# Optimization experiments

Measured on AMD Instinct MI355X. Metric: run time of the kernel, lower is better.

Reference implementation:

```python
import jax, jax.numpy as jnp
import numpy as np

C, H, W, D, M = 64, 512, 512, 4, 16


def setup_inputs() -> dict:
    key = jax.random.key(0)
    ks = jax.random.split(key, 9)
    scale = (1.0 / (C * C)) ** 0.5
    return {
        "q": jax.random.normal(ks[0], (1, 1, H, W), jnp.float32),
        "proj_w": jax.random.normal(ks[1], (C, 1, 1, 1), jnp.float32),
        "proj_b": jax.random.normal(ks[2], (C, 1, 1), jnp.float32) * 0.01,
        "spec_wr": jax.random.normal(ks[3], (D, C, C, M, M), jnp.float32) * scale,
        "spec_wi": jax.random.normal(ks[4], (D, C, C, M, M), jnp.float32) * scale,
        "w_w": jax.random.normal(ks[5], (D, C, C, 1, 1), jnp.float32) * (1.0 / C ** 0.5),
        "w_b": jax.random.normal(ks[6], (D, C, 1, 1), jnp.float32) * 0.01,
        "final_w": jax.random.normal(ks[7], (1, C, 1, 1), jnp.float32) * (1.0 / C ** 0.5),
        "final_b": jax.random.normal(ks[8], (1, 1, 1), jnp.float32) * 0.01,
    }


def _spectral(x, wr, wi, m):
    # x: (C,H,W). FFT2 -> contract low modes -> zero-pad -> iFFT2, take real part.
    Cin, Hh, Ww = x.shape
    x_ft = jnp.fft.fft2(x, axes=(-2, -1))  # (C,H,W) complex
    w = (wr + 1j * wi).astype(x_ft.dtype)  # (Cin,Cout,m,m)
    out_sub = jnp.einsum('imn,iomn->omn', x_ft[:, :m, :m], w)
    out_ft = jnp.zeros((wr.shape[1], Hh, Ww), dtype=x_ft.dtype).at[:, :m, :m].set(out_sub)
    return jnp.fft.ifft2(out_ft, axes=(-2, -1)).real


def reference(q, proj_w, proj_b, spec_wr, spec_wi, w_w, w_b, final_w, final_b):
    m = spec_wr.shape[-1]
    depth = spec_wr.shape[0]
    x = q[0].astype(jnp.float32)  # (C_in,H,W) -- batch must be 1
    # 1x1 conv lift
    x = jnp.einsum('oi,ihw->ohw', proj_w[:, :, 0, 0], x) + proj_b
    for d in range(depth):
        x_spec = _spectral(x, spec_wr[d], spec_wi[d], m)
        x_local = jnp.einsum('oi,ihw->ohw', w_w[d, :, :, 0, 0], x) + w_b[d]
        x = jax.nn.gelu(x_spec + x_local)
    x = jnp.einsum('oi,ihw->ohw', final_w[:, :, 0, 0], x) + final_b
    return x[None]  # re-add batch dim
```

## Files before the change

### kernel.cpp

```cpp
#include <hip/hip_runtime.h>
#include <cmath>

#define CC 64
#define HH 512
#define WWID 512
#define HWSZ (HH*WWID)
#define DEPTH 4

typedef __attribute__((ext_vector_type(8))) short short8;
typedef __attribute__((ext_vector_type(4))) float floatx4;

__device__ inline unsigned short f2bf(float f){
  unsigned int u = __float_as_uint(f);
  u += 0x7FFF + ((u >> 16) & 1);
  return (unsigned short)(u >> 16);
}
__device__ inline float bf2f(unsigned short h){
  return __uint_as_float(((unsigned int)h) << 16);
}

__global__ void k_init(const float* __restrict__ ww,
                       float* __restrict__ ctab, float* __restrict__ stab,
                       unsigned short* __restrict__ trigBh, unsigned short* __restrict__ trigBl,
                       unsigned short* __restrict__ trigTh, unsigned short* __restrict__ trigTl,
                       unsigned short* __restrict__ Whi, unsigned short* __restrict__ Wlo,
                       float4* __restrict__ Xfz){
  if (blockIdx.x < 32) Xfz[blockIdx.x*256 + threadIdx.x] = make_float4(0.f,0.f,0.f,0.f);
  int idx = blockIdx.x*256 + threadIdx.x;
  if (idx < 8192){
    int pos = idx >> 4, k = idx & 15;
    int r = (pos * k) & 511;
    double ang = (2.0 * 3.14159265358979323846 / 512.0) * (double)r;
    float c = (float)cos(ang), s = (float)sin(ang);
    ctab[idx] = c;  stab[idx] = s;
    unsigned short ch = f2bf(c), sh = f2bf(s);
    unsigned short cl = f2bf(c - bf2f(ch)), sl = f2bf(s - bf2f(sh));
    trigBh[pos*32 + 2*k]     = ch;  trigBl[pos*32 + 2*k]     = cl;
    trigBh[pos*32 + 2*k + 1] = sh;  trigBl[pos*32 + 2*k + 1] = sl;
    trigTh[(2*k)*512 + pos]   = ch;  trigTl[(2*k)*512 + pos]   = cl;
    trigTh[(2*k+1)*512 + pos] = sh;  trigTl[(2*k+1)*512 + pos] = sl;
  } else {
    int t = idx - 8192;
    float v = ww[t];
    unsigned short h = f2bf(v);
    Whi[t] = h;  Wlo[t] = f2bf(v - bf2f(h));
  }
}

#define APITCH 136
#define XPITCH 33
template<int LIFT>
__global__ __launch_bounds__(256) void k_dftw(const float* __restrict__ x,
    const float* __restrict__ qsrc, const float* __restrict__ pw, const float* __restrict__ pb,
    const unsigned short* __restrict__ trigTh, const unsigned short* __restrict__ trigTl,
    const float* __restrict__ ctab, const float* __restrict__ stab,
    float* __restrict__ Xfa, float4* __restrict__ Yz){
  if (blockIdx.x < 32) Yz[blockIdx.x*256 + threadIdx.x] = make_float4(0.f,0.f,0.f,0.f);

  __shared__ unsigned short Ahs[64*APITCH], Als[64*APITCH];
  __shared__ unsigned short Bhs[32*APITCH], Bls[32*APITCH];
  __shared__ float X1s[64*XPITCH];
  int row0 = blockIdx.x * 64;
  int i  = row0 >> 9;
  int h0 = row0 & 511;
  int t = threadIdx.x;
  int g = t >> 6, lm = t & 15, lq = (t >> 4) & 3;
  float pa = 0.f, pbv = 0.f;
  if (LIFT){ pa = pw[i]; pbv = pb[i]; }

  floatx4 acc[2] = {{0.f,0.f,0.f,0.f},{0.f,0.f,0.f,0.f}};

  for (int kc = 0; kc < 4; ++kc){
    {
      int r = t >> 2, qq = t & 3;
      const float4* src4 = LIFT
        ? (const float4*)(qsrc + (size_t)(h0 + r)*512 + kc*128 + qq*32)
        : (const float4*)(x    + (size_t)(row0 + r)*512 + kc*128 + qq*32);
      unsigned int* dh = (unsigned int*)&Ahs[r*APITCH + qq*32];
      unsigned int* dl = (unsigned int*)&Als[r*APITCH + qq*32];
      #pragma unroll
      for (int u = 0; u < 8; ++u){
        float4 v = src4[u];
        if (LIFT){
          v.x = fmaf(pa, v.x, pbv); v.y = fmaf(pa, v.y, pbv);
          v.z = fmaf(pa, v.z, pbv); v.w = fmaf(pa, v.w, pbv);
        }
        unsigned short h0_ = f2bf(v.x), h1 = f2bf(v.y), h2 = f2bf(v.z), h3 = f2bf(v.w);
        dh[u*2]   = (unsigned)h0_ | ((unsigned)h1 << 16);
        dh[u*2+1] = (unsigned)h2 | ((unsigned)h3 << 16);
        unsigned short g0 = f2bf(v.x - bf2f(h0_)), g1 = f2bf(v.y - bf2f(h1));
        unsigned short g2 = f2bf(v.z - bf2f(h2)), g3 = f2bf(v.w - bf2f(h3));
        dl[u*2]   = (unsigned)g0 | ((unsigned)g1 << 16);
        dl[u*2+1] = (unsigned)g2 | ((unsigned)g3 << 16);
      }
    }
    {
      int j = t >> 3, qq = t & 7;
      const unsigned int* sh = (const unsigned int*)trigTh + j*256 + kc*64 + qq*8;
      const unsigned int* sl = (const unsigned int*)trigTl + j*256 + kc*64 + qq*8;
      unsigned int* dh = (unsigned int*)&Bhs[j*APITCH + qq*16];
      unsigned int* dl = (unsigned int*)&Bls[j*APITCH + qq*16];
      #pragma unroll
      for (int u = 0; u < 8; ++u){ dh[u] = sh[u]; dl[u] = sl[u]; }
    }
    __syncthreads();
    #pragma unroll
    for (int ks = 0; ks < 4; ++ks){
      short8 ah = *(const short8*)&Ahs[(g*16 + lm)*APITCH + ks*32 + lq*8];
      short8 al = *(const short8*)&Als[(g*16 + lm)*APITCH + ks*32 + lq*8];
      #pragma unroll
      for (int nt = 0; nt < 2; ++nt){
        short8 bh = *(const short8*)&Bhs[(nt*16 + lm)*APITCH + ks*32 + lq*8];
        short8 bl = *(const short8*)&Bls[(nt*16 + lm)*APITCH + ks*32 + lq*8];
        acc[nt] = __builtin_amdgcn_mfma_f32_16x16x32_bf16(ah, bh, acc[nt], 0, 0, 0);
        acc[nt] = __builtin_amdgcn_mfma_f32_16x16x32_bf16(ah, bl, acc[nt], 0, 0, 0);
        acc[nt] = __builtin_amdgcn_mfma_f32_16x16x32_bf16(al, bh, acc[nt], 0, 0, 0);
      }
    }
    __syncthreads();
  }
  #pragma unroll
  for (int nt = 0; nt < 2; ++nt){
    int j = nt*16 + lm;
    float sgn = (j & 1) ? -1.f : 1.f;
    #pragma unroll
    for (int rg = 0; rg < 4; ++rg){
      int m = g*16 + lq*4 + rg;
      X1s[m*XPITCH + j] = sgn * acc[nt][rg];
    }
  }
  __syncthreads();

  int mo = t >> 4, n = t & 15;
  float ar = 0.f, ai = 0.f;
  #pragma unroll 8
  for (int hh = 0; hh < 64; ++hh){
    int h = h0 + hh;
    float Re = X1s[hh*XPITCH + 2*n];
    float Im = X1s[hh*XPITCH + 2*n + 1];
    float c = ctab[h*16 + mo], s = stab[h*16 + mo];
    ar += Re*c + Im*s;
    ai += Im*c - Re*s;
  }
  atomicAdd(&Xfa[(i*256 + t)*2],     ar);
  atomicAdd(&Xfa[(i*256 + t)*2 + 1], ai);
}

__global__ void k_contract(const float2* __restrict__ Xf,
                           const float* __restrict__ wr, const float* __restrict__ wi,
                           float* __restrict__ Ya){
  int o = blockIdx.x, ic = blockIdx.y;
  int mn = blockIdx.z*64 + threadIdx.x;
  float ar = 0.f, ai = 0.f;
  int i0 = ic * 16;
  #pragma unroll
  for (int ii = 0; ii < 16; ++ii){
    int i = i0 + ii;
    float2 xf = Xf[i*256 + mn];
    float wrv = wr[(i*64 + o)*256 + mn];
    float wiv = wi[(i*64 + o)*256 + mn];
    ar += xf.x*wrv - xf.y*wiv;
    ai += xf.x*wiv + xf.y*wrv;
  }
  const float sc = 1.f/262144.f;
  atomicAdd(&Ya[(o*256 + mn)*2],     ar*sc);
  atomicAdd(&Ya[(o*256 + mn)*2 + 1], ai*sc);
}

__global__ void k_idfth(const float2* __restrict__ Y, const float* __restrict__ ct,
                        const float* __restrict__ st,
                        unsigned int* __restrict__ Thi, unsigned int* __restrict__ Tlo,
                        float4* __restrict__ Xfz){
  if (blockIdx.x < 32) Xfz[blockIdx.x*256 + threadIdx.x] = make_float4(0.f,0.f,0.f,0.f);
  int idx = blockIdx.x*256 + threadIdx.x;
  int n = idx & 15, o = (idx >> 4) & 63, h = idx >> 10;
  float ar = 0.f, ai = 0.f;
  #pragma unroll
  for (int m = 0; m < 16; ++m){
    float2 y = Y[(o<<8) + (m<<4) + n];
    float c = ct[h*16 + m], s = st[h*16 + m];
    ar += y.x*c - y.y*s;
    ai += y.x*s + y.y*c;
  }
  float tr = ar, ts = -ai;
  unsigned short rh = f2bf(tr), sh = f2bf(ts);
  Thi[idx] = (unsigned int)rh | ((unsigned int)sh << 16);
  unsigned short rl = f2bf(tr - bf2f(rh)), slr = f2bf(ts - bf2f(sh));
  Tlo[idx] = (unsigned int)rl | ((unsigned int)slr << 16);
}

#define PITCH 104
template<int LIFT, int FINAL>
__global__ __launch_bounds__(256) void k_combine(
    const float* __restrict__ x, const float* __restrict__ qsrc,
    const float* __restrict__ pw, const float* __restrict__ pb,
    const unsigned short* __restrict__ Whid, const unsigned short* __restrict__ Wlod,
    const unsigned int* __restrict__ Thi,  const unsigned int* __restrict__ Tlo,
    const unsigned short* __restrict__ trigBh, const unsigned short* __restrict__ trigBl,
    const float* __restrict__ wb, float* __restrict__ xo,
    const float* __restrict__ fw, const float* __restrict__ fb,
    float* __restrict__ outp)
{
  __shared__ unsigned short Ah[64*PITCH],  Al[64*PITCH];
  __shared__ unsigned short Bh[128*PITCH], Bl[128*PITCH];
  int h  = blockIdx.y;
  int w0 = blockIdx.x * 128;
  int t  = threadIdx.x;

  {
    int wl = t & 127, ig = t >> 7;
    if (LIFT){
      float qv = qsrc[(size_t)h*512 + w0 + wl];
      #pragma unroll
      for (int ii = 0; ii < 32; ii += 2){
        int i0 = ig*32 + ii;
        float v0 = fmaf(pw[i0],   qv, pb[i0]);
        float v1 = fmaf(pw[i0+1], qv, pb[i0+1]);
        unsigned short h0 = f2bf(v0), h1 = f2bf(v1);
        unsigned short g0 = f2bf(v0 - bf2f(h0)), g1 = f2bf(v1 - bf2f(h1));
        *(unsigned int*)&Bh[wl*PITCH + i0] = (unsigned int)h0 | ((unsigned int)h1 << 16);
        *(unsigned int*)&Bl[wl*PITCH + i0] = (unsigned int)g0 | ((unsigned int)g1 << 16);
      }
    } else {
      const float* xb = x + (size_t)h*512 + w0 + wl;
      #pragma unroll
      for (int ii = 0; ii < 32; ii += 2){
        int i0 = ig*32 + ii;
        float v0 = xb[(size_t)i0*HWSZ];
        float v1 = xb[(size_t)(i0+1)*HWSZ];
        unsigned short h0 = f2bf(v0), h1 = f2bf(v1);
        unsigned short g0 = f2bf(v0 - bf2f(h0)), g1 = f2bf(v1 - bf2f(h1));
        *(unsigned int*)&Bh[wl*PITCH + i0] = (unsigned int)h0 | ((unsigned int)h1 << 16);
        *(unsigned int*)&Bl[wl*PITCH + i0] = (unsigned int)g0 | ((unsigned int)g1 << 16);
      }
    }
  }
  {
    int row = t >> 1, qq = t & 1;
    const unsigned int* sh = (const unsigned int*)trigBh + (size_t)(w0+row)*16 + qq*8;
    const unsigned int* sl = (const unsigned int*)trigBl + (size_t)(w0+row)*16 + qq*8;
    unsigned int* dh = (unsigned int*)&Bh[row*PITCH + 64] + qq*8;
    unsigned int* dl = (unsigned int*)&Bl[row*PITCH + 64] + qq*8;
    #pragma unroll
    for (int u = 0; u < 8; ++u){ dh[u] = sh[u]; dl[u] = sl[u]; }
  }
  {
    int o = t >> 2, q8 = t & 3;
    const unsigned int* sh = (const unsigned int*)Whid + o*32 + q8*8;
    const unsigned int* sl = (const unsigned int*)Wlod + o*32 + q8*8;
    unsigned int* dh = (unsigned int*)&Ah[o*PITCH] + q8*8;
    unsigned int* dl = (unsigned int*)&Al[o*PITCH] + q8*8;
    #pragma unroll
    for (int u = 0; u < 8; ++u){ dh[u] = sh[u]; dl[u] = sl[u]; }
  }
  {
    int o = t >> 2, q4 = t & 3;
    const unsigned int* sh = Thi + (size_t)h*1024 + o*16 + q4*4;
    const unsigned int* sl = Tlo + (size_t)h*1024 + o*16 + q4*4;
    unsigned int* dh = (unsigned int*)&Ah[o*PITCH + 64] + q4*4;
    unsigned int* dl = (unsigned int*)&Al[o*PITCH + 64] + q4*4;
    #pragma unroll
    for (int u = 0; u < 4; ++u){ dh[u] = sh[u]; dl[u] = sl[u]; }
  }
  __syncthreads();

  int g  = t >> 6;
  int lm = t & 15;
  int lq = (t >> 4) & 3;

  floatx4 acc[8] = {{0.f,0.f,0.f,0.f},{0.f,0.f,0.f,0.f},{0.f,0.f,0.f,0.f},{0.f,0.f,0.f,0.f},
                    {0.f,0.f,0.f,0.f},{0.f,0.f,0.f,0.f},{0.f,0.f,0.f,0.f},{0.f,0.f,0.f,0.f}};

  #pragma unroll
  for (int ks = 0; ks < 3; ++ks){
    short8 af = *(const short8*)&Ah[(g*16 + lm)*PITCH + ks*32 + lq*8];
    short8 al = *(const short8*)&Al[(g*16 + lm)*PITCH + ks*32 + lq*8];
    #pragma unroll
    for (int nt = 0; nt < 8; ++nt){
      short8 bf = *(const short8*)&Bh[(nt*16 + lm)*PITCH + ks*32 + lq*8];
      short8 bl = *(const short8*)&Bl[(nt*16 + lm)*PITCH + ks*32 + lq*8];
      acc[nt] = __builtin_amdgcn_mfma_f32_16x16x32_bf16(af, bf, acc[nt], 0, 0, 0);
      acc[nt] = __builtin_amdgcn_mfma_f32_16x16x32_bf16(af, bl, acc[nt], 0, 0, 0);
      acc[nt] = __builtin_amdgcn_mfma_f32_16x16x32_bf16(al, bf, acc[nt], 0, 0, 0);
    }
  }

  if (!FINAL){
    #pragma unroll
    for (int nt = 0; nt < 8; ++nt){
      int w = w0 + nt*16 + lm;
      #pragma unroll
      for (int rg = 0; rg < 4; ++rg){
        int o = g*16 + lq*4 + rg;
        float u = acc[nt][rg] + wb[o];
        float z = 0.7978845608028654f * fmaf(0.044715f, u*u*u, u);
        float e = __expf(2.f*z);
        float gl = u - __fdividef(u, e + 1.f);
        xo[(size_t)o*HWSZ + (size_t)h*512 + w] = gl;
      }
    }
  } else {
    float* fred = (float*)Ah;
    __syncthreads();
    #pragma unroll
    for (int nt = 0; nt < 8; ++nt){
      float partial = 0.f;
      #pragma unroll
      for (int rg = 0; rg < 4; ++rg){
        int o = g*16 + lq*4 + rg;
        float u = acc[nt][rg] + wb[o];
        float z = 0.7978845608028654f * fmaf(0.044715f, u*u*u, u);
        float e = __expf(2.f*z);
        float gl = u - __fdividef(u, e + 1.f);
        partial = fmaf(fw[o], gl, partial);
      }
      fred[(nt*16 + lm)*17 + (t >> 4)] = partial;
    }
    __syncthreads();
    if (t < 128){
      float s = fb[0];
      #pragma unroll
      for (int k2 = 0; k2 < 16; ++k2) s += fred[t*17 + k2];
      outp[(size_t)h*512 + w0 + t] = s;
    }
  }
}

extern "C" void kernel_launch(void* const* d_in, const int* in_sizes, int n_in,
                              void* d_out, int out_size, void* d_ws, size_t ws_size,
                              hipStream_t stream) {
  const float* q       = (const float*)d_in[0];
  const float* proj_w  = (const float*)d_in[1];
  const float* proj_b  = (const float*)d_in[2];
  const float* spec_wr = (const float*)d_in[3];
  const float* spec_wi = (const float*)d_in[4];
  const float* w_w     = (const float*)d_in[5];
  const float* w_b     = (const float*)d_in[6];
  const float* final_w = (const float*)d_in[7];
  const float* final_b = (const float*)d_in[8];
  float* out = (float*)d_out;

  char* ws = (char*)d_ws;
  float*  ctab = (float*) (ws + 0);
  float*  stab = (float*) (ws + 32768);
  unsigned short* trigBh = (unsigned short*)(ws + 65536);
  unsigned short* trigBl = (unsigned short*)(ws + 98304);
  unsigned int* Thi = (unsigned int*)(ws + 131072);
  unsigned int* Tlo = (unsigned int*)(ws + 2228224);
  float*  Xf   = (float*) (ws + 4325376);
  float*  Y    = (float*) (ws + 4456448);
  float*  x    = (float*) (ws + 4587520);
  unsigned short* Whi = (unsigned short*)(ws + 71696384);
  unsigned short* Wlo = (unsigned short*)(ws + 71729152);
  unsigned short* trigTh = (unsigned short*)(ws + 71761920);
  unsigned short* trigTl = (unsigned short*)(ws + 71794688);

  k_init<<<96, 256, 0, stream>>>(w_w, ctab, stab, trigBh, trigBl, trigTh, trigTl,
                                 Whi, Wlo, (float4*)Xf);

  for (int d = 0; d < DEPTH; ++d){
    if (d == 0)
      k_dftw<1><<<512, 256, 0, stream>>>(x, q, proj_w, proj_b, trigTh, trigTl,
                                         ctab, stab, Xf, (float4*)Y);
    else
      k_dftw<0><<<512, 256, 0, stream>>>(x, q, proj_w, proj_b, trigTh, trigTl,
                                         ctab, stab, Xf, (float4*)Y);
    k_contract<<<dim3(64,4,4), 64, 0, stream>>>((const float2*)Xf,
                                                spec_wr + (size_t)d*1048576,
                                                spec_wi + (size_t)d*1048576, Y);
    k_idfth<<<2048, 256, 0, stream>>>((const float2*)Y, ctab, stab, Thi, Tlo,
                                      (float4*)Xf);
    if (d == 0)
      k_combine<1,0><<<dim3(4,512), 256, 0, stream>>>(x, q, proj_w, proj_b,
          Whi + d*4096, Wlo + d*4096, Thi, Tlo, trigBh, trigBl,
          w_b + d*64, x, final_w, final_b, out);
    else if (d < DEPTH-1)
      k_combine<0,0><<<dim3(4,512), 256, 0, stream>>>(x, q, proj_w, proj_b,
          Whi + d*4096, Wlo + d*4096, Thi, Tlo, trigBh, trigBl,
          w_b + d*64, x, final_w, final_b, out);
    else
      k_combine<0,1><<<dim3(4,512), 256, 0, stream>>>(x, q, proj_w, proj_b,
          Whi + d*4096, Wlo + d*4096, Thi, Tlo, trigBh, trigBl,
          w_b + d*64, x, final_w, final_b, out);
  }
}
```

Baseline: 322.2 us.

## Store activations as packed bf16 hi/lo pairs and vectorize shared-memory staging

The combine kernel now writes each activation as a packed 32-bit word holding its bf16 high and low split, in place of fp32. Both consumers, the DFT and combine kernels, read this packed form and only shuffle bits instead of recomputing the hi/lo split. This removes the repeated float-to-bf16 conversion work in every layer. Shared-memory staging copies are also widened to uint2/uint4 accesses. Memory traffic is unchanged because the word is still 32 bits. Numerically it matches the previous split, so accuracy should be preserved.

```diff
diff --git a/kernel.cpp b/kernel.cpp
--- a/kernel.cpp
+++ b/kernel.cpp
@@ -50,7 +50,7 @@
 #define APITCH 136
 #define XPITCH 33
 template<int LIFT>
-__global__ __launch_bounds__(256) void k_dftw(const float* __restrict__ x,
+__global__ __launch_bounds__(256) void k_dftw(const unsigned int* __restrict__ xp,
     const float* __restrict__ qsrc, const float* __restrict__ pw, const float* __restrict__ pb,
     const unsigned short* __restrict__ trigTh, const unsigned short* __restrict__ trigTl,
     const float* __restrict__ ctab, const float* __restrict__ stab,
@@ -73,35 +73,49 @@
   for (int kc = 0; kc < 4; ++kc){
     {
       int r = t >> 2, qq = t & 3;
-      const float4* src4 = LIFT
-        ? (const float4*)(qsrc + (size_t)(h0 + r)*512 + kc*128 + qq*32)
-        : (const float4*)(x    + (size_t)(row0 + r)*512 + kc*128 + qq*32);
       unsigned int* dh = (unsigned int*)&Ahs[r*APITCH + qq*32];
       unsigned int* dl = (unsigned int*)&Als[r*APITCH + qq*32];
-      #pragma unroll
-      for (int u = 0; u < 8; ++u){
-        float4 v = src4[u];
-        if (LIFT){
+      if (LIFT){
+        const float4* src4 = (const float4*)(qsrc + (size_t)(h0 + r)*512 + kc*128 + qq*32);
+        #pragma unroll
+        for (int u = 0; u < 8; ++u){
+          float4 v = src4[u];
           v.x = fmaf(pa, v.x, pbv); v.y = fmaf(pa, v.y, pbv);
           v.z = fmaf(pa, v.z, pbv); v.w = fmaf(pa, v.w, pbv);
+          unsigned short h0_ = f2bf(v.x), h1 = f2bf(v.y), h2 = f2bf(v.z), h3 = f2bf(v.w);
+          unsigned short g0 = f2bf(v.x - bf2f(h0_)), g1 = f2bf(v.y - bf2f(h1));
+          unsigned short g2 = f2bf(v.z - bf2f(h2)), g3 = f2bf(v.w - bf2f(h3));
+          uint2 ph, pl;
+          ph.x = (unsigned)h0_ | ((unsigned)h1 << 16);
+          ph.y = (unsigned)h2 | ((unsigned)h3 << 16);
+          pl.x = (unsigned)g0 | ((unsigned)g1 << 16);
+          pl.y = (unsigned)g2 | ((unsigned)g3 << 16);
+          *(uint2*)&dh[u*2] = ph;
+          *(uint2*)&dl[u*2] = pl;
         }
-        unsigned short h0_ = f2bf(v.x), h1 = f2bf(v.y), h2 = f2bf(v.z), h3 = f2bf(v.w);
-        dh[u*2]   = (unsigned)h0_ | ((unsigned)h1 << 16);
-        dh[u*2+1] = (unsigned)h2 | ((unsigned)h3 << 16);
-        unsigned short g0 = f2bf(v.x - bf2f(h0_)), g1 = f2bf(v.y - bf2f(h1));
-        unsigned short g2 = f2bf(v.z - bf2f(h2)), g3 = f2bf(v.w - bf2f(h3));
-        dl[u*2]   = (unsigned)g0 | ((unsigned)g1 << 16);
-        dl[u*2+1] = (unsigned)g2 | ((unsigned)g3 << 16);
+      } else {
+        const uint4* srcp = (const uint4*)(xp + (size_t)(row0 + r)*512 + kc*128 + qq*32);
+        #pragma unroll
+        for (int u = 0; u < 8; ++u){
+          uint4 v = srcp[u];
+          uint2 ph, pl;
+          ph.x = (v.x & 0xffffu) | (v.y << 16);
+          ph.y = (v.z & 0xffffu) | (v.w << 16);
+          pl.x = (v.x >> 16) | (v.y & 0xffff0000u);
+          pl.y = (v.z >> 16) | (v.w & 0xffff0000u);
+          *(uint2*)&dh[u*2] = ph;
+          *(uint2*)&dl[u*2] = pl;
+        }
       }
     }
     {
       int j = t >> 3, qq = t & 7;
-      const unsigned int* sh = (const unsigned int*)trigTh + j*256 + kc*64 + qq*8;
-      const unsigned int* sl = (const unsigned int*)trigTl + j*256 + kc*64 + qq*8;
-      unsigned int* dh = (unsigned int*)&Bhs[j*APITCH + qq*16];
-      unsigned int* dl = (unsigned int*)&Bls[j*APITCH + qq*16];
-      #pragma unroll
-      for (int u = 0; u < 8; ++u){ dh[u] = sh[u]; dl[u] = sl[u]; }
+      const uint4* sh = (const uint4*)((const unsigned int*)trigTh + j*256 + kc*64 + qq*8);
+      const uint4* sl = (const uint4*)((const unsigned int*)trigTl + j*256 + kc*64 + qq*8);
+      uint4* dh = (uint4*)&Bhs[j*APITCH + qq*16];
+      uint4* dl = (uint4*)&Bls[j*APITCH + qq*16];
+      dh[0] = sh[0]; dh[1] = sh[1];
+      dl[0] = sl[0]; dl[1] = sl[1];
     }
     __syncthreads();
     #pragma unroll
@@ -192,12 +206,12 @@
 #define PITCH 104
 template<int LIFT, int FINAL>
 __global__ __launch_bounds__(256) void k_combine(
-    const float* __restrict__ x, const float* __restrict__ qsrc,
+    const unsigned int* __restrict__ xp, const float* __restrict__ qsrc,
     const float* __restrict__ pw, const float* __restrict__ pb,
     const unsigned short* __restrict__ Whid, const unsigned short* __restrict__ Wlod,
     const unsigned int* __restrict__ Thi,  const unsigned int* __restrict__ Tlo,
     const unsigned short* __restrict__ trigBh, const unsigned short* __restrict__ trigBl,
-    const float* __restrict__ wb, float* __restrict__ xo,
+    const float* __restrict__ wb, unsigned int* __restrict__ xo,
     const float* __restrict__ fw, const float* __restrict__ fb,
     float* __restrict__ outp)
 {
@@ -212,55 +226,68 @@
     if (LIFT){
       float qv = qsrc[(size_t)h*512 + w0 + wl];
       #pragma unroll
-      for (int ii = 0; ii < 32; ii += 2){
+      for (int ii = 0; ii < 32; ii += 4){
         int i0 = ig*32 + ii;
         float v0 = fmaf(pw[i0],   qv, pb[i0]);
         float v1 = fmaf(pw[i0+1], qv, pb[i0+1]);
-        unsigned short h0 = f2bf(v0), h1 = f2bf(v1);
+        float v2 = fmaf(pw[i0+2], qv, pb[i0+2]);
+        float v3 = fmaf(pw[i0+3], qv, pb[i0+3]);
+        unsigned short h0 = f2bf(v0), h1 = f2bf(v1), h2 = f2bf(v2), h3 = f2bf(v3);
         unsigned short g0 = f2bf(v0 - bf2f(h0)), g1 = f2bf(v1 - bf2f(h1));
-        *(unsigned int*)&Bh[wl*PITCH + i0] = (unsigned int)h0 | ((unsigned int)h1 << 16);
-        *(unsigned int*)&Bl[wl*PITCH + i0] = (unsigned int)g0 | ((unsigned int)g1 << 16);
+        unsigned short g2 = f2bf(v2 - bf2f(h2)), g3 = f2bf(v3 - bf2f(h3));
+        uint2 ph, pl;
+        ph.x = (unsigned)h0 | ((unsigned)h1 << 16);
+        ph.y = (unsigned)h2 | ((unsigned)h3 << 16);
+        pl.x = (unsigned)g0 | ((unsigned)g1 << 16);
+        pl.y = (unsigned)g2 | ((unsigned)g3 << 16);
+        *(uint2*)&Bh[wl*PITCH + i0] = ph;
+        *(uint2*)&Bl[wl*PITCH + i0] = pl;
       }
     } else {
-      const float* xb = x + (size_t)h*512 + w0 + wl;
-      #pragma unroll
-      for (int ii = 0; ii < 32; ii += 2){
+      const unsigned int* xb = xp + (size_t)h*512 + w0 + wl;
+      #pragma unroll
+      for (int ii = 0; ii < 32; ii += 4){
         int i0 = ig*32 + ii;
-        float v0 = xb[(size_t)i0*HWSZ];
-        float v1 = xb[(size_t)(i0+1)*HWSZ];
-        unsigned short h0 = f2bf(v0), h1 = f2bf(v1);
-        unsigned short g0 = f2bf(v0 - bf2f(h0)), g1 = f2bf(v1 - bf2f(h1));
-        *(unsigned int*)&Bh[wl*PITCH + i0] = (unsigned int)h0 | ((unsigned int)h1 << 16);
-        *(unsigned int*)&Bl[wl*PITCH + i0] = (unsigned int)g0 | ((unsigned int)g1 << 16);
+        unsigned int v0 = xb[(size_t)(i0  )*HWSZ];
+        unsigned int v1 = xb[(size_t)(i0+1)*HWSZ];
+        unsigned int v2 = xb[(size_t)(i0+2)*HWSZ];
+        unsigned int v3 = xb[(size_t)(i0+3)*HWSZ];
+        uint2 ph, pl;
+        ph.x = (v0 & 0xffffu) | (v1 << 16);
+        ph.y = (v2 & 0xffffu) | (v3 << 16);
+        pl.x = (v0 >> 16) | (v1 & 0xffff0000u);
+        pl.y = (v2 >> 16) | (v3 & 0xffff0000u);
+        *(uint2*)&Bh[wl*PITCH + i0] = ph;
+        *(uint2*)&Bl[wl*PITCH + i0] = pl;
       }
     }
   }
   {
     int row = t >> 1, qq = t & 1;
-    const unsigned int* sh = (const unsigned int*)trigBh + (size_t)(w0+row)*16 + qq*8;
-    const unsigned int* sl = (const unsigned int*)trigBl + (size_t)(w0+row)*16 + qq*8;
-    unsigned int* dh = (unsigned int*)&Bh[row*PITCH + 64] + qq*8;
-    unsigned int* dl = (unsigned int*)&Bl[row*PITCH + 64] + qq*8;
-    #pragma unroll
-    for (int u = 0; u < 8; ++u){ dh[u] = sh[u]; dl[u] = sl[u]; }
+    const uint4* sh = (const uint4*)((const unsigned int*)trigBh + (size_t)(w0+row)*16 + qq*8);
+    const uint4* sl = (const uint4*)((const unsigned int*)trigBl + (size_t)(w0+row)*16 + qq*8);
+    uint4* dh = (uint4*)((unsigned int*)&Bh[row*PITCH + 64] + qq*8);
+    uint4* dl = (uint4*)((unsigned int*)&Bl[row*PITCH + 64] + qq*8);
+    dh[0] = sh[0]; dh[1] = sh[1];
+    dl[0] = sl[0]; dl[1] = sl[1];
   }
   {
     int o = t >> 2, q8 = t & 3;
-    const unsigned int* sh = (const unsigned int*)Whid + o*32 + q8*8;
-    const unsigned int* sl = (const unsigned int*)Wlod + o*32 + q8*8;
-    unsigned int* dh = (unsigned int*)&Ah[o*PITCH] + q8*8;
-    unsigned int* dl = (unsigned int*)&Al[o*PITCH] + q8*8;
-    #pragma unroll
-    for (int u = 0; u < 8; ++u){ dh[u] = sh[u]; dl[u] = sl[u]; }
+    const uint4* sh = (const uint4*)((const unsigned int*)Whid + o*32 + q8*8);
+    const uint4* sl = (const uint4*)((const unsigned int*)Wlod + o*32 + q8*8);
+    uint4* dh = (uint4*)((unsigned int*)&Ah[o*PITCH] + q8*8);
+    uint4* dl = (uint4*)((unsigned int*)&Al[o*PITCH] + q8*8);
+    dh[0] = sh[0]; dh[1] = sh[1];
+    dl[0] = sl[0]; dl[1] = sl[1];
   }
   {
     int o = t >> 2, q4 = t & 3;
-    const unsigned int* sh = Thi + (size_t)h*1024 + o*16 + q4*4;
-    const unsigned int* sl = Tlo + (size_t)h*1024 + o*16 + q4*4;
-    unsigned int* dh = (unsigned int*)&Ah[o*PITCH + 64] + q4*4;
-    unsigned int* dl = (unsigned int*)&Al[o*PITCH + 64] + q4*4;
-    #pragma unroll
-    for (int u = 0; u < 4; ++u){ dh[u] = sh[u]; dl[u] = sl[u]; }
+    const uint4* sh = (const uint4*)(Thi + (size_t)h*1024 + o*16 + q4*4);
+    const uint4* sl = (const uint4*)(Tlo + (size_t)h*1024 + o*16 + q4*4);
+    uint4* dh = (uint4*)((unsigned int*)&Ah[o*PITCH + 64] + q4*4);
+    uint4* dl = (uint4*)((unsigned int*)&Al[o*PITCH + 64] + q4*4);
+    dh[0] = sh[0];
+    dl[0] = sl[0];
   }
   __syncthreads();
 
@@ -296,7 +323,9 @@
         float z = 0.7978845608028654f * fmaf(0.044715f, u*u*u, u);
         float e = __expf(2.f*z);
         float gl = u - __fdividef(u, e + 1.f);
-        xo[(size_t)o*HWSZ + (size_t)h*512 + w] = gl;
+        unsigned short hi_ = f2bf(gl);
+        unsigned short lo_ = f2bf(gl - bf2f(hi_));
+        xo[(size_t)o*HWSZ + (size_t)h*512 + w] = (unsigned int)hi_ | ((unsigned int)lo_ << 16);
       }
     }
   } else {
@@ -349,7 +378,7 @@
   unsigned int* Tlo = (unsigned int*)(ws + 2228224);
   float*  Xf   = (float*) (ws + 4325376);
   float*  Y    = (float*) (ws + 4456448);
-  float*  x    = (float*) (ws + 4587520);
+  unsigned int* x = (unsigned int*)(ws + 4587520);
   unsigned short* Whi = (unsigned short*)(ws + 71696384);
   unsigned short* Wlo = (unsigned short*)(ws + 71729152);
   unsigned short* trigTh = (unsigned short*)(ws + 71761920);
```

Result: slower. 329.0 us (+2.1%).
